# Kernel tuning notes

Hardware: AMD Instinct MI355X
Metric: run time of the kernel (lower is better)

Reference implementation:

```python
import jax, jax.numpy as jnp
import numpy as np

B, CI, H, W = 16, 32, 224, 224
CO, K, STRIDE = 32, 3, 1


def setup_inputs() -> dict:
    key = jax.random.key(0)
    k1, k2, k3 = jax.random.split(key, 3)
    x = jax.random.normal(k1, (B, CI, H, W), dtype=jnp.float32)
    weights = jax.random.normal(k2, (CO, CI, K, K), dtype=jnp.float32)
    bias = jax.random.normal(k3, (CO,), dtype=jnp.float32)
    return {"x": x, "weights": weights, "bias": bias}


def reference(x, weights, bias):
    # Faithful to HandmadeConv2D with padding=0, stride=1: a VALID
    # cross-correlation (the torch code never actually pads x) plus bias.
    out = jax.lax.conv_general_dilated(
        x, weights,
        window_strides=(STRIDE, STRIDE),
        padding="VALID",
        dimension_numbers=("NCHW", "OIHW", "NCHW"),
    )
    return out + bias[None, :, None, None]
```

## Files before the change

### kernel.cpp

```cpp
#include <hip/hip_runtime.h>
#include <hip/hip_bf16.h>

#define B_  16
#define CI_ 32
#define H_  224
#define W_  224
#define CO_ 32
#define OH_ 222
#define OW_ 222
#define HW_ (H_*W_)
#define K_  288

#define OHB   8
#define ROWS  10
#define OWT   64
#define PXT   66
#define NOHB  28
#define NOWT  4
#define NPAIR (ROWS*(PXT/2))
#define NBLK  (NOHB*NOWT*B_)

typedef __attribute__((ext_vector_type(8))) short short8;
typedef __attribute__((ext_vector_type(4))) float float4v;
typedef float float4u __attribute__((ext_vector_type(4), aligned(4)));

__device__ __forceinline__ unsigned swz(unsigned L) {
    return L ^ (((L >> 7) & 7u) << 4);
}

__global__ void wprep(const float* __restrict__ w, unsigned short* __restrict__ wbf) {
    int idx = blockIdx.x * 256 + threadIdx.x;
    if (idx >= CO_ * K_) return;
    int co  = idx / K_;
    int rem = idx - co * K_;
    int ci  = rem / 9;
    int g   = rem - ci * 9;
    unsigned int u = __float_as_uint(w[idx]);
    u = u + 0x7FFFu + ((u >> 16) & 1u);
    wbf[co * K_ + g * 32 + ci] = (unsigned short)(u >> 16);
}

__global__ __launch_bounds__(512, 6) void conv_fused(
    const float* __restrict__ x, const unsigned short* __restrict__ wbf,
    const float* __restrict__ bias, float* __restrict__ out)
{
    __shared__ unsigned short Xs[ROWS * PXT * CI_];

    const int t   = threadIdx.x;
    const int bid = blockIdx.x;
    const int xcd   = bid & 7;
    const int owt   = (bid >> 3) & 3;
    const int gid   = (bid >> 5) * 8 + xcd;
    const int b     = gid / NOHB;
    const int ohblk = gid - b * NOHB;
    const int r0    = ohblk * OHB;
    const int ow0   = owt * OWT;

    if (t < NPAIR) {
        const int tr = t / (PXT / 2);
        const int j  = t - tr * (PXT / 2);
        int row = r0 + tr;  if (row > H_ - 1) row = H_ - 1;
        const int c = ow0 + 2 * j;
        const float* xp = x + (size_t)b * CI_ * HW_ + (size_t)row * W_;
        const unsigned base = (unsigned)(tr * PXT + 2 * j) * 64u;
#pragma unroll
        for (int h = 0; h < 2; ++h) {
            float2 f2[16];
            if (c + 1 < W_) {
#pragma unroll
                for (int i = 0; i < 16; ++i)
                    f2[i] = *(const float2*)&xp[(size_t)(h * 16 + i) * HW_ + c];
            } else {
#pragma unroll
                for (int i = 0; i < 16; ++i) {
                    float s = xp[(size_t)(h * 16 + i) * HW_ + (W_ - 1)];
                    f2[i] = make_float2(s, s);
                }
            }
            union { short8 s8[4]; __hip_bfloat162 h2[16]; } u;
#pragma unroll
            for (int i = 0; i < 8; ++i) {
                u.h2[i]     = __float22bfloat162_rn(make_float2(f2[2*i].x, f2[2*i+1].x));
                u.h2[8 + i] = __float22bfloat162_rn(make_float2(f2[2*i].y, f2[2*i+1].y));
            }
#pragma unroll
            for (int q2 = 0; q2 < 4; ++q2) {
                const int cc = (q2 < 2) ? (2 * h + q2) : (4 + 2 * h + (q2 - 2));
                *(short8*)((char*)Xs + swz(base + (unsigned)cc * 16u)) = u.s8[q2];
            }
        }
    }
    __syncthreads();

    const int lane = t & 63;
    const int wv   = t >> 6;
    const int oh   = r0 + wv;
    if (oh >= OH_) return;
    const int i16  = lane & 15;
    const int quad = lane >> 4;

    const unsigned short* wr0 = wbf + (size_t)i16 * K_;
    const unsigned short* wr1 = wbf + (size_t)(16 + i16) * K_;

    float4v acc[4][2] = {};

#pragma unroll
    for (int g = 0; g < 9; ++g) {
        const int kh = g / 3;
        const int kw = g - kh * 3;
        const short8 b0 = *(const short8*)&wr0[g * 32 + quad * 8];
        const short8 b1 = *(const short8*)&wr1[g * 32 + quad * 8];
        const unsigned rowbase = (unsigned)((wv + kh) * PXT) * 64u + (unsigned)quad * 16u;
#pragma unroll
        for (int ot = 0; ot < 4; ++ot) {
            const unsigned L = rowbase + (unsigned)(ot * 16 + i16 + kw) * 64u;
            const short8 a = *(const short8*)((const char*)Xs + swz(L));
            acc[ot][0] = __builtin_amdgcn_mfma_f32_16x16x32_bf16(a, b0, acc[ot][0], 0, 0, 0);
            acc[ot][1] = __builtin_amdgcn_mfma_f32_16x16x32_bf16(a, b1, acc[ot][1], 0, 0, 0);
        }
    }

    const float bv0 = bias[i16];
    const float bv1 = bias[16 + i16];
    const size_t o0 = ((size_t)(b * CO_ + i16) * OH_ + oh) * (size_t)OW_;
    const size_t o1 = ((size_t)(b * CO_ + 16 + i16) * OH_ + oh) * (size_t)OW_;
#pragma unroll
    for (int ot = 0; ot < 4; ++ot) {
        const int owq = ow0 + ot * 16 + quad * 4;
        float4u v0 = { acc[ot][0][0] + bv0, acc[ot][0][1] + bv0,
                       acc[ot][0][2] + bv0, acc[ot][0][3] + bv0 };
        float4u v1 = { acc[ot][1][0] + bv1, acc[ot][1][1] + bv1,
                       acc[ot][1][2] + bv1, acc[ot][1][3] + bv1 };
        if (owq + 3 < OW_) {
            *(float4u*)&out[o0 + owq] = v0;
            *(float4u*)&out[o1 + owq] = v1;
        } else {
#pragma unroll
            for (int r = 0; r < 4; ++r) {
                if (owq + r < OW_) {
                    out[o0 + owq + r] = acc[ot][0][r] + bv0;
                    out[o1 + owq + r] = acc[ot][1][r] + bv1;
                }
            }
        }
    }
}

extern "C" void kernel_launch(void* const* d_in, const int* in_sizes, int n_in,
                              void* d_out, int out_size, void* d_ws, size_t ws_size,
                              hipStream_t stream) {
    const float* x    = (const float*)d_in[0];
    const float* w    = (const float*)d_in[1];
    const float* bias = (const float*)d_in[2];
    float* out        = (float*)d_out;
    unsigned short* wbf = (unsigned short*)d_ws;

    wprep<<<(CO_ * K_ + 255) / 256, 256, 0, stream>>>(w, wbf);
    conv_fused<<<dim3(NBLK), 512, 0, stream>>>(x, wbf, bias, out);
}
```

Baseline: 223.5 us.

## Stream input rows through a 10-slot LDS ring with software prefetch

Each block now processes a 20-row chunk of output rows in steps of 4 with 256 threads. Input rows sit in a ring buffer of 10 LDS slots, and the next 4 rows are loaded into registers while the MFMAs for the current step run. This cuts the redundant halo loads of the old 8-row blocks (10 input rows per 8 output rows) and overlaps global loads with compute. The cost is fewer blocks, more registers for the 32 float2 prefetch values, and a barrier on every step.

```diff
diff --git a/kernel.cpp b/kernel.cpp
--- a/kernel.cpp
+++ b/kernel.cpp
@@ -1,24 +1,24 @@
 #include <hip/hip_runtime.h>
 #include <hip/hip_bf16.h>
 
-#define B_  16
-#define CI_ 32
-#define H_  224
-#define W_  224
-#define CO_ 32
-#define OH_ 222
-#define OW_ 222
-#define HW_ (H_*W_)
-#define K_  288
+#define B_   16
+#define CI_  32
+#define H_   224
+#define W_   224
+#define CO_  32
+#define OH_  222
+#define OW_  222
+#define HW_  (H_*W_)
+#define K_   288
 
-#define OHB   8
-#define ROWS  10
-#define OWT   64
-#define PXT   66
-#define NOHB  28
-#define NOWT  4
-#define NPAIR (ROWS*(PXT/2))
-#define NBLK  (NOHB*NOWT*B_)
+#define OWTW   64
+#define PXT_   66
+#define NPAIR  33
+#define RING   10
+#define SLABB  (PXT_*CI_*2)
+#define CHROWS 20
+#define NCHUNK 12
+#define NBLK   (NCHUNK*4*B_)
 
 typedef __attribute__((ext_vector_type(8))) short short8;
 typedef __attribute__((ext_vector_type(4))) float float4v;
@@ -26,6 +26,12 @@
 
 __device__ __forceinline__ unsigned swz(unsigned L) {
     return L ^ (((L >> 7) & 7u) << 4);
+}
+
+__device__ __forceinline__ int wrap10(int v) {
+    if (v >= 20) return v - 20;
+    if (v >= 10) return v - 10;
+    return v;
 }
 
 __global__ void wprep(const float* __restrict__ w, unsigned short* __restrict__ wbf) {
@@ -40,109 +46,130 @@
     wbf[co * K_ + g * 32 + ci] = (unsigned short)(u >> 16);
 }
 
-__global__ __launch_bounds__(512, 6) void conv_fused(
+__device__ __forceinline__ void load_pair(const float* __restrict__ xp, int c, float2* f2) {
+    if (c + 1 < W_) {
+#pragma unroll
+        for (int i = 0; i < 32; ++i)
+            f2[i] = *(const float2*)&xp[(size_t)i * HW_ + c];
+    } else {
+#pragma unroll
+        for (int i = 0; i < 32; ++i) {
+            float v = xp[(size_t)i * HW_ + (W_ - 1)];
+            f2[i] = make_float2(v, v);
+        }
+    }
+}
+
+__device__ __forceinline__ void cvt_write_pair(unsigned short* Xs, int slot, int j,
+                                               const float2* f2) {
+    union { short8 s8[8]; __hip_bfloat162 h2[32]; } u;
+#pragma unroll
+    for (int i = 0; i < 16; ++i) {
+        u.h2[i]      = __float22bfloat162_rn(make_float2(f2[2*i].x, f2[2*i+1].x));
+        u.h2[16 + i] = __float22bfloat162_rn(make_float2(f2[2*i].y, f2[2*i+1].y));
+    }
+    const unsigned base = (unsigned)(slot * NPAIR + j) * 128u;
+#pragma unroll
+    for (int k = 0; k < 8; ++k)
+        *(short8*)((char*)Xs + swz(base + (unsigned)k * 16u)) = u.s8[k];
+}
+
+__global__ __launch_bounds__(256, 3) void conv_fused(
     const float* __restrict__ x, const unsigned short* __restrict__ wbf,
     const float* __restrict__ bias, float* __restrict__ out)
 {
-    __shared__ unsigned short Xs[ROWS * PXT * CI_];
+    __shared__ unsigned short Xs[RING * PXT_ * CI_];
 
     const int t   = threadIdx.x;
     const int bid = blockIdx.x;
     const int xcd   = bid & 7;
     const int owt   = (bid >> 3) & 3;
     const int gid   = (bid >> 5) * 8 + xcd;
-    const int b     = gid / NOHB;
-    const int ohblk = gid - b * NOHB;
-    const int r0    = ohblk * OHB;
-    const int ow0   = owt * OWT;
+    const int b     = gid / NCHUNK;
+    const int chunk = gid - b * NCHUNK;
+    const int r0    = chunk * CHROWS;
+    const int ow0   = owt * OWTW;
+    const int NS    = min(5, (OH_ - r0 + 3) >> 2);
 
-    if (t < NPAIR) {
-        const int tr = t / (PXT / 2);
-        const int j  = t - tr * (PXT / 2);
-        int row = r0 + tr;  if (row > H_ - 1) row = H_ - 1;
-        const int c = ow0 + 2 * j;
-        const float* xp = x + (size_t)b * CI_ * HW_ + (size_t)row * W_;
-        const unsigned base = (unsigned)(tr * PXT + 2 * j) * 64u;
-#pragma unroll
-        for (int h = 0; h < 2; ++h) {
-            float2 f2[16];
-            if (c + 1 < W_) {
-#pragma unroll
-                for (int i = 0; i < 16; ++i)
-                    f2[i] = *(const float2*)&xp[(size_t)(h * 16 + i) * HW_ + c];
-            } else {
-#pragma unroll
-                for (int i = 0; i < 16; ++i) {
-                    float s = xp[(size_t)(h * 16 + i) * HW_ + (W_ - 1)];
-                    f2[i] = make_float2(s, s);
-                }
-            }
-            union { short8 s8[4]; __hip_bfloat162 h2[16]; } u;
-#pragma unroll
-            for (int i = 0; i < 8; ++i) {
-                u.h2[i]     = __float22bfloat162_rn(make_float2(f2[2*i].x, f2[2*i+1].x));
-                u.h2[8 + i] = __float22bfloat162_rn(make_float2(f2[2*i].y, f2[2*i+1].y));
-            }
-#pragma unroll
-            for (int q2 = 0; q2 < 4; ++q2) {
-                const int cc = (q2 < 2) ? (2 * h + q2) : (4 + 2 * h + (q2 - 2));
-                *(short8*)((char*)Xs + swz(base + (unsigned)cc * 16u)) = u.s8[q2];
-            }
-        }
+    const int lane = t & 63, wv = t >> 6;
+    const int i16  = lane & 15, quad = lane >> 4;
+
+    const float* xb = x + (size_t)b * CI_ * HW_;
+
+    float2 f2[32];
+
+    if (t < 6 * NPAIR) {
+        const int tr = t / NPAIR, j = t - tr * NPAIR;
+        int gr = r0 + tr; if (gr > H_ - 1) gr = H_ - 1;
+        load_pair(xb + (size_t)gr * W_, ow0 + 2 * j, f2);
+        cvt_write_pair(Xs, tr, j, f2);
     }
     __syncthreads();
 
-    const int lane = t & 63;
-    const int wv   = t >> 6;
-    const int oh   = r0 + wv;
-    if (oh >= OH_) return;
-    const int i16  = lane & 15;
-    const int quad = lane >> 4;
-
+    const float bv0 = bias[i16];
+    const float bv1 = bias[16 + i16];
     const unsigned short* wr0 = wbf + (size_t)i16 * K_;
     const unsigned short* wr1 = wbf + (size_t)(16 + i16) * K_;
 
-    float4v acc[4][2] = {};
+    const int s_tr = t / NPAIR;
+    const int s_j  = t - s_tr * NPAIR;
+    const int s_c  = ow0 + 2 * s_j;
 
+    for (int s = 0; s < NS; ++s) {
+        const bool pref = (t < 4 * NPAIR) && (s + 1 < NS);
+        int slotW = 0;
+        if (pref) {
+            const int gr0 = r0 + 4 * s + 6 + s_tr;
+            slotW = wrap10(4 * s + 6 + s_tr);
+            const int gr = gr0 > H_ - 1 ? H_ - 1 : gr0;
+            load_pair(xb + (size_t)gr * W_, s_c, f2);
+        }
+        __builtin_amdgcn_sched_barrier(0);
+
+        const int oh = r0 + 4 * s + wv;
+        if (oh < OH_) {
+            float4v acc[4][2] = {};
+            const int sl0 = 4 * s + wv;
 #pragma unroll
-    for (int g = 0; g < 9; ++g) {
-        const int kh = g / 3;
-        const int kw = g - kh * 3;
-        const short8 b0 = *(const short8*)&wr0[g * 32 + quad * 8];
-        const short8 b1 = *(const short8*)&wr1[g * 32 + quad * 8];
-        const unsigned rowbase = (unsigned)((wv + kh) * PXT) * 64u + (unsigned)quad * 16u;
+            for (int g = 0; g < 9; ++g) {
+                const int kh = g / 3, kw = g - kh * 3;
+                const int sl = wrap10(sl0 + kh);
+                const short8 b0 = *(const short8*)&wr0[g * 32 + quad * 8];
+                const short8 b1 = *(const short8*)&wr1[g * 32 + quad * 8];
+                const unsigned rowbase = (unsigned)(sl * SLABB) + (unsigned)quad * 16u;
 #pragma unroll
-        for (int ot = 0; ot < 4; ++ot) {
-            const unsigned L = rowbase + (unsigned)(ot * 16 + i16 + kw) * 64u;
-            const short8 a = *(const short8*)((const char*)Xs + swz(L));
-            acc[ot][0] = __builtin_amdgcn_mfma_f32_16x16x32_bf16(a, b0, acc[ot][0], 0, 0, 0);
-            acc[ot][1] = __builtin_amdgcn_mfma_f32_16x16x32_bf16(a, b1, acc[ot][1], 0, 0, 0);
-        }
-    }
-
-    const float bv0 = bias[i16];
-    const float bv1 = bias[16 + i16];
-    const size_t o0 = ((size_t)(b * CO_ + i16) * OH_ + oh) * (size_t)OW_;
-    const size_t o1 = ((size_t)(b * CO_ + 16 + i16) * OH_ + oh) * (size_t)OW_;
+                for (int ot = 0; ot < 4; ++ot) {
+                    const unsigned L = rowbase + (unsigned)(ot * 16 + i16 + kw) * 64u;
+                    const short8 a = *(const short8*)((const char*)Xs + swz(L));
+                    acc[ot][0] = __builtin_amdgcn_mfma_f32_16x16x32_bf16(a, b0, acc[ot][0], 0, 0, 0);
+                    acc[ot][1] = __builtin_amdgcn_mfma_f32_16x16x32_bf16(a, b1, acc[ot][1], 0, 0, 0);
+                }
+            }
+            const size_t o0 = ((size_t)(b * CO_ + i16) * OH_ + oh) * (size_t)OW_;
+            const size_t o1 = ((size_t)(b * CO_ + 16 + i16) * OH_ + oh) * (size_t)OW_;
 #pragma unroll
-    for (int ot = 0; ot < 4; ++ot) {
-        const int owq = ow0 + ot * 16 + quad * 4;
-        float4u v0 = { acc[ot][0][0] + bv0, acc[ot][0][1] + bv0,
-                       acc[ot][0][2] + bv0, acc[ot][0][3] + bv0 };
-        float4u v1 = { acc[ot][1][0] + bv1, acc[ot][1][1] + bv1,
-                       acc[ot][1][2] + bv1, acc[ot][1][3] + bv1 };
-        if (owq + 3 < OW_) {
-            *(float4u*)&out[o0 + owq] = v0;
-            *(float4u*)&out[o1 + owq] = v1;
-        } else {
+            for (int ot = 0; ot < 4; ++ot) {
+                const int owq = ow0 + ot * 16 + quad * 4;
+                float4u v0 = { acc[ot][0][0] + bv0, acc[ot][0][1] + bv0,
+                               acc[ot][0][2] + bv0, acc[ot][0][3] + bv0 };
+                float4u v1 = { acc[ot][1][0] + bv1, acc[ot][1][1] + bv1,
+                               acc[ot][1][2] + bv1, acc[ot][1][3] + bv1 };
+                if (owq + 3 < OW_) {
+                    *(float4u*)&out[o0 + owq] = v0;
+                    *(float4u*)&out[o1 + owq] = v1;
+                } else {
 #pragma unroll
-            for (int r = 0; r < 4; ++r) {
-                if (owq + r < OW_) {
-                    out[o0 + owq + r] = acc[ot][0][r] + bv0;
-                    out[o1 + owq + r] = acc[ot][1][r] + bv1;
+                    for (int r = 0; r < 4; ++r)
+                        if (owq + r < OW_) {
+                            out[o0 + owq + r] = acc[ot][0][r] + bv0;
+                            out[o1 + owq + r] = acc[ot][1][r] + bv1;
+                        }
                 }
             }
         }
+
+        if (pref) cvt_write_pair(Xs, slotW, s_j, f2);
+        __syncthreads();
     }
 }
 
@@ -156,5 +183,5 @@
     unsigned short* wbf = (unsigned short*)d_ws;
 
     wprep<<<(CO_ * K_ + 255) / 256, 256, 0, stream>>>(w, wbf);
-    conv_fused<<<dim3(NBLK), 512, 0, stream>>>(x, wbf, bias, out);
+    conv_fused<<<dim3(NBLK), 256, 0, stream>>>(x, wbf, bias, out);
 }
```

After: 233.9 us. 1.05x slower.
